# Performance work log

Hardware: AMD Instinct MI355X
Metric: run time of the kernel (lower is better)

Reference implementation:

```python
import jax, jax.numpy as jnp
import numpy as np

BINS = 8

def setup_inputs() -> dict:
    key = jax.random.key(0)
    k1, k2, k3 = jax.random.split(key, 3)
    B, H, W = 32, 160, 160
    HW = H * W
    reg_logits = jax.random.normal(k1, (B, 4 * BINS, H, W), dtype=jnp.float32)
    targets = jax.random.uniform(k2, (B, HW, 4), dtype=jnp.float32) * (BINS - 1)
    pos_mask = jax.random.randint(k3, (B, HW), 0, 2) == 1
    return {"reg_logits": reg_logits, "targets": targets, "pos_mask": pos_mask}

def reference(reg_logits, targets, pos_mask):
    bins = BINS
    B, C, H, W = reg_logits.shape
    HW = H * W
    # [B, C, H, W] -> [B, HW, 4, bins]
    rl = reg_logits.transpose(0, 2, 3, 1).reshape(B, HW, 4, bins)
    t = jnp.clip(targets, 0.0, bins - 1 - 0.0001)          # [B, HW, 4]
    l_id = jnp.floor(t).astype(jnp.int32)
    u_id = jnp.minimum(l_id + 1, bins - 1)
    w_u = t - l_id.astype(t.dtype)
    w_l = 1.0 - w_u
    logp = jax.nn.log_softmax(rl, axis=-1)                 # [B, HW, 4, bins]
    nll_l = -jnp.take_along_axis(logp, l_id[..., None], axis=-1)[..., 0]
    nll_u = -jnp.take_along_axis(logp, u_id[..., None], axis=-1)[..., 0]
    per = w_l * nll_l + w_u * nll_u                        # [B, HW, 4]
    m = pos_mask.astype(per.dtype)                         # [B, HW]
    npos = jnp.sum(m)
    # mean over positives per coordinate, averaged over 4 coords ==
    # sum over (positives x 4) / (npos * 4)
    total = jnp.sum(per * m[..., None])
    loss = total / (jnp.maximum(npos, 1.0) * 4.0)
    return jnp.where(npos > 0, loss, jnp.zeros((), dtype=per.dtype))
```

## Files before the change

kernel.cpp:

```cpp
#include <hip/hip_runtime.h>

#define BINS 8
#define BLOCK 256

constexpr int BATCH   = 32;
constexpr int HW      = 25600;
constexpr int NPIX    = BATCH * HW;
constexpr int NGROUPS = NPIX / 4;
constexpr int GPB     = 64;
constexpr int NBLOCKS = NGROUPS / GPB;

__device__ __forceinline__ float comp4(const float4& v, int i) {
    return (i == 0) ? v.x : (i == 1) ? v.y : (i == 2) ? v.z : v.w;
}

__global__ __launch_bounds__(BLOCK, 8) void dfl_main_kernel(
    const float* __restrict__ logits,
    const float* __restrict__ targets,
    const int*   __restrict__ mask,
    float* __restrict__ partials) {

    const int lane = threadIdx.x & 63;
    const int c    = threadIdx.x >> 6;
    const int g    = blockIdx.x * GPB + lane;
    const int p4   = g << 2;
    const int b    = p4 / HW;
    const int pp   = p4 - b * HW;

    const float* base = logits + ((size_t)b * 4 * BINS + (size_t)c * BINS) * HW + pp;

    float4 xv[BINS];
#pragma unroll
    for (int j = 0; j < BINS; ++j)
        xv[j] = *(const float4*)(base + (size_t)j * HW);

    float tc[4];
#pragma unroll
    for (int i = 0; i < 4; ++i)
        tc[i] = targets[(size_t)(p4 + i) * 4 + c];

    const int4 mk = *(const int4*)(mask + p4);
    float msk[4];
    msk[0] = mk.x ? 1.0f : 0.0f;
    msk[1] = mk.y ? 1.0f : 0.0f;
    msk[2] = mk.z ? 1.0f : 0.0f;
    msk[3] = mk.w ? 1.0f : 0.0f;

    float tsum = 0.0f;
    float tcnt = msk[0] + msk[1] + msk[2] + msk[3];

#pragma unroll
    for (int i = 0; i < 4; ++i) {
        float t = fminf(fmaxf(tc[i], 0.0f), (float)(BINS - 1) - 0.0001f);
        float lf = floorf(t);
        int   li = (int)lf;
        float wu = t - lf;
        float wl = 1.0f - wu;

        float s = 0.0f;
#pragma unroll
        for (int j = 0; j < BINS; ++j) s += __expf(comp4(xv[j], i));
        float lse = __logf(s);

        float xl = comp4(xv[0], i);
        float xu = comp4(xv[1], i);
#pragma unroll
        for (int j = 1; j < BINS; ++j) xl = (li == j)     ? comp4(xv[j], i) : xl;
#pragma unroll
        for (int j = 2; j < BINS; ++j) xu = (li == j - 1) ? comp4(xv[j], i) : xu;

        tsum += msk[i] * (lse - (wl * xl + wu * xu));
    }

#pragma unroll
    for (int off = 32; off > 0; off >>= 1) {
        tsum += __shfl_down(tsum, off, 64);
        tcnt += __shfl_down(tcnt, off, 64);
    }

    __shared__ float ssum[BLOCK / 64];
    __shared__ float scnt[BLOCK / 64];
    if (lane == 0) { ssum[c] = tsum; scnt[c] = tcnt; }
    __syncthreads();
    if (threadIdx.x == 0) {
        float bs = 0.0f, bc = 0.0f;
#pragma unroll
        for (int w = 0; w < BLOCK / 64; ++w) { bs += ssum[w]; bc += scnt[w]; }
        partials[2 * blockIdx.x]     = bs;
        partials[2 * blockIdx.x + 1] = bc;
    }
}

__global__ __launch_bounds__(BLOCK) void finalize_kernel(
    const float* __restrict__ partials, float* __restrict__ out) {

    float tsum = 0.0f, tcnt = 0.0f;
    for (int i = threadIdx.x; i < NBLOCKS; i += BLOCK) {
        tsum += partials[2 * i];
        tcnt += partials[2 * i + 1];
    }
#pragma unroll
    for (int off = 32; off > 0; off >>= 1) {
        tsum += __shfl_down(tsum, off, 64);
        tcnt += __shfl_down(tcnt, off, 64);
    }
    __shared__ float ssum[BLOCK / 64];
    __shared__ float scnt[BLOCK / 64];
    const int wid  = threadIdx.x >> 6;
    const int lane = threadIdx.x & 63;
    if (lane == 0) { ssum[wid] = tsum; scnt[wid] = tcnt; }
    __syncthreads();
    if (threadIdx.x == 0) {
        float total = 0.0f, npos4 = 0.0f;
#pragma unroll
        for (int w = 0; w < BLOCK / 64; ++w) { total += ssum[w]; npos4 += scnt[w]; }
        float loss = total / fmaxf(npos4, 1.0f);
        out[0] = (npos4 > 0.0f) ? loss : 0.0f;
    }
}

extern "C" void kernel_launch(void* const* d_in, const int* in_sizes, int n_in,
                              void* d_out, int out_size, void* d_ws, size_t ws_size,
                              hipStream_t stream) {
    const float* logits  = (const float*)d_in[0];
    const float* targets = (const float*)d_in[1];
    const int*   mask    = (const int*)d_in[2];
    float* out      = (float*)d_out;
    float* partials = (float*)d_ws;

    dfl_main_kernel<<<NBLOCKS, BLOCK, 0, stream>>>(logits, targets, mask, partials);
    finalize_kernel<<<1, BLOCK, 0, stream>>>(partials, out);
}
```

Before: 167.6 us.

## Assign one pixel per thread and widen finalize reduction block

The main kernel now gives each thread one pixel instead of four, loading scalar floats in place of float4 vectors. This launches four times as many blocks, which cuts per-thread register use and raises memory-level parallelism. Block partials are stored as float2, and the finalize kernel uses 1024 threads to reduce the now four-times-larger partial array. The trade-off is narrower per-thread loads and more blocks and partials to reduce.

```diff
diff --git a/kernel.cpp b/kernel.cpp
--- a/kernel.cpp
+++ b/kernel.cpp
@@ -2,75 +2,58 @@
 
 #define BINS 8
 #define BLOCK 256
+#define FBLOCK 1024
 
-constexpr int BATCH   = 32;
-constexpr int HW      = 25600;
-constexpr int NPIX    = BATCH * HW;
-constexpr int NGROUPS = NPIX / 4;
-constexpr int GPB     = 64;
-constexpr int NBLOCKS = NGROUPS / GPB;
-
-__device__ __forceinline__ float comp4(const float4& v, int i) {
-    return (i == 0) ? v.x : (i == 1) ? v.y : (i == 2) ? v.z : v.w;
-}
+constexpr int BATCH       = 32;
+constexpr int HW          = 25600;
+constexpr int NPIX        = BATCH * HW;
+constexpr int PIX_PER_BLK = 64;
+constexpr int NBLOCKS     = NPIX / PIX_PER_BLK;
 
 __global__ __launch_bounds__(BLOCK, 8) void dfl_main_kernel(
     const float* __restrict__ logits,
     const float* __restrict__ targets,
     const int*   __restrict__ mask,
-    float* __restrict__ partials) {
+    float2* __restrict__ partials) {
 
-    const int lane = threadIdx.x & 63;
-    const int c    = threadIdx.x >> 6;
-    const int g    = blockIdx.x * GPB + lane;
-    const int p4   = g << 2;
-    const int b    = p4 / HW;
-    const int pp   = p4 - b * HW;
+    const int tid     = threadIdx.x;
+    const int lane    = tid & 63;
+    const int c       = tid >> 6;
+    const int pixbase = blockIdx.x * PIX_PER_BLK;
+    const int pix     = pixbase + lane;
 
-    const float* base = logits + ((size_t)b * 4 * BINS + (size_t)c * BINS) * HW + pp;
+    const int b  = pixbase / HW;
+    const int pp = pixbase - b * HW;
 
-    float4 xv[BINS];
+    const float* base =
+        logits + (size_t)(b * 4 * BINS + c * BINS) * HW + pp + lane;
+
+    float x[BINS];
 #pragma unroll
-    for (int j = 0; j < BINS; ++j)
-        xv[j] = *(const float4*)(base + (size_t)j * HW);
+    for (int j = 0; j < BINS; ++j) x[j] = base[(size_t)j * HW];
 
-    float tc[4];
+    float t = targets[(size_t)pix * 4 + c];
+    const float m = mask[pix] ? 1.0f : 0.0f;
+
+    t = fminf(fmaxf(t, 0.0f), (float)(BINS - 1) - 0.0001f);
+    const float lf = floorf(t);
+    const int   li = (int)lf;
+    const float wu = t - lf;
+    const float wl = 1.0f - wu;
+
+    float s = 0.0f;
 #pragma unroll
-    for (int i = 0; i < 4; ++i)
-        tc[i] = targets[(size_t)(p4 + i) * 4 + c];
+    for (int j = 0; j < BINS; ++j) s += __expf(x[j]);
+    const float lse = __logf(s);
 
-    const int4 mk = *(const int4*)(mask + p4);
-    float msk[4];
-    msk[0] = mk.x ? 1.0f : 0.0f;
-    msk[1] = mk.y ? 1.0f : 0.0f;
-    msk[2] = mk.z ? 1.0f : 0.0f;
-    msk[3] = mk.w ? 1.0f : 0.0f;
+    float xl = x[0], xu = x[1];
+#pragma unroll
+    for (int j = 1; j < BINS; ++j) xl = (li == j)     ? x[j] : xl;
+#pragma unroll
+    for (int j = 2; j < BINS; ++j) xu = (li == j - 1) ? x[j] : xu;
 
-    float tsum = 0.0f;
-    float tcnt = msk[0] + msk[1] + msk[2] + msk[3];
-
-#pragma unroll
-    for (int i = 0; i < 4; ++i) {
-        float t = fminf(fmaxf(tc[i], 0.0f), (float)(BINS - 1) - 0.0001f);
-        float lf = floorf(t);
-        int   li = (int)lf;
-        float wu = t - lf;
-        float wl = 1.0f - wu;
-
-        float s = 0.0f;
-#pragma unroll
-        for (int j = 0; j < BINS; ++j) s += __expf(comp4(xv[j], i));
-        float lse = __logf(s);
-
-        float xl = comp4(xv[0], i);
-        float xu = comp4(xv[1], i);
-#pragma unroll
-        for (int j = 1; j < BINS; ++j) xl = (li == j)     ? comp4(xv[j], i) : xl;
-#pragma unroll
-        for (int j = 2; j < BINS; ++j) xu = (li == j - 1) ? comp4(xv[j], i) : xu;
-
-        tsum += msk[i] * (lse - (wl * xl + wu * xu));
-    }
+    float tsum = m * (lse - (wl * xl + wu * xu));
+    float tcnt = m;
 
 #pragma unroll
     for (int off = 32; off > 0; off >>= 1) {
@@ -82,30 +65,30 @@
     __shared__ float scnt[BLOCK / 64];
     if (lane == 0) { ssum[c] = tsum; scnt[c] = tcnt; }
     __syncthreads();
-    if (threadIdx.x == 0) {
+    if (tid == 0) {
         float bs = 0.0f, bc = 0.0f;
 #pragma unroll
         for (int w = 0; w < BLOCK / 64; ++w) { bs += ssum[w]; bc += scnt[w]; }
-        partials[2 * blockIdx.x]     = bs;
-        partials[2 * blockIdx.x + 1] = bc;
+        partials[blockIdx.x] = make_float2(bs, bc);
     }
 }
 
-__global__ __launch_bounds__(BLOCK) void finalize_kernel(
-    const float* __restrict__ partials, float* __restrict__ out) {
+__global__ __launch_bounds__(FBLOCK) void finalize_kernel(
+    const float2* __restrict__ partials, float* __restrict__ out) {
 
     float tsum = 0.0f, tcnt = 0.0f;
-    for (int i = threadIdx.x; i < NBLOCKS; i += BLOCK) {
-        tsum += partials[2 * i];
-        tcnt += partials[2 * i + 1];
+    for (int i = threadIdx.x; i < NBLOCKS; i += FBLOCK) {
+        const float2 p = partials[i];
+        tsum += p.x;
+        tcnt += p.y;
     }
 #pragma unroll
     for (int off = 32; off > 0; off >>= 1) {
         tsum += __shfl_down(tsum, off, 64);
         tcnt += __shfl_down(tcnt, off, 64);
     }
-    __shared__ float ssum[BLOCK / 64];
-    __shared__ float scnt[BLOCK / 64];
+    __shared__ float ssum[FBLOCK / 64];
+    __shared__ float scnt[FBLOCK / 64];
     const int wid  = threadIdx.x >> 6;
     const int lane = threadIdx.x & 63;
     if (lane == 0) { ssum[wid] = tsum; scnt[wid] = tcnt; }
@@ -113,8 +96,10 @@
     if (threadIdx.x == 0) {
         float total = 0.0f, npos4 = 0.0f;
 #pragma unroll
-        for (int w = 0; w < BLOCK / 64; ++w) { total += ssum[w]; npos4 += scnt[w]; }
-        float loss = total / fmaxf(npos4, 1.0f);
+        for (int w = 0; w < FBLOCK / 64; ++w) {
+            total += ssum[w]; npos4 += scnt[w];
+        }
+        const float loss = total / fmaxf(npos4, 1.0f);
         out[0] = (npos4 > 0.0f) ? loss : 0.0f;
     }
 }
@@ -125,9 +110,9 @@
     const float* logits  = (const float*)d_in[0];
     const float* targets = (const float*)d_in[1];
     const int*   mask    = (const int*)d_in[2];
-    float* out      = (float*)d_out;
-    float* partials = (float*)d_ws;
+    float* out       = (float*)d_out;
+    float2* partials = (float2*)d_ws;
 
     dfl_main_kernel<<<NBLOCKS, BLOCK, 0, stream>>>(logits, targets, mask, partials);
-    finalize_kernel<<<1, BLOCK, 0, stream>>>(partials, out);
+    finalize_kernel<<<1, FBLOCK, 0, stream>>>(partials, out);
 }
```

Result: no change. 168.7 us (+0.7%).
